# Kernel optimization log

Measured on AMD Instinct MI355X. Metric: run time of the kernel, lower is better.

The kernel has to match this reference:

```python
import jax, jax.numpy as jnp
import numpy as np

EPS = 1e-6

def elu_feature_map(x):
    return jax.nn.elu(x) + 1.0

def setup_inputs() -> dict:
    key = jax.random.key(0)
    kq, kk, kv = jax.random.split(key, 3)
    N, L, S, H, D = 8, 8192, 8192, 8, 32
    queries = jax.random.normal(kq, (N, L, H, D), dtype=jnp.float32)
    keys = jax.random.normal(kk, (N, S, H, D), dtype=jnp.float32)
    values = jax.random.normal(kv, (N, S, H, D), dtype=jnp.float32)
    return {"queries": queries, "keys": keys, "values": values}

def reference(queries, keys, values):
    # Linear attention ("Transformers are RNNs"), ELU+1 feature map.
    Q = elu_feature_map(queries)            # [N, L, H, D]
    K = elu_feature_map(keys)               # [N, S, H, D]
    v_length = values.shape[1]
    v = values / v_length                   # [N, S, H, D]
    # KV = sum_s K_s (outer) V_s  -> [N, H, D, D] (fused, no per-token outer products)
    KV = jnp.einsum('nshd,nshv->nhdv', K, v)
    # Normalizer: Z = 1 / (Q . sum_s K_s + eps)  -> [N, L, H]
    K_sum = K.sum(axis=1)                   # [N, H, D]
    Z = 1.0 / (jnp.einsum('nlhd,nhd->nlh', Q, K_sum) + EPS)
    # out = (Q @ KV) * Z * v_length  -> [N, L, H, D]
    out = jnp.einsum('nlhd,nhdv->nlhv', Q, KV) * Z[..., None] * v_length
    return out
```

## Files before the change

### kernel.cpp

```cpp
#include <hip/hip_runtime.h>
#include <hip/hip_bf16.h>


#define NN 8
#define LL 8192
#define SS 8192
#define HH 8
#define DD 32
#define HD (HH*DD)
#define EPSF 1e-6f

#define KV_FLOATS (NN*HH*DD*DD)
#define KS_FLOATS (NN*HH*DD)
#define FINAL_FLOATS (KV_FLOATS + KS_FLOATS)

#define P1_CHUNKS 64
#define P1_BLOCKS (NN*P1_CHUNKS)
#define P1_CS (SS/P1_CHUNKS)
#define P1_TS 8
#define PBLK 8448

#define P2_TS 8
#define P2_LB 64
#define P2_CHUNKS (LL/P2_LB)

__device__ __forceinline__ float elu1(float x) {
    return x > 0.f ? x + 1.f : __expf(x);
}

template<bool ATOMIC>
__global__ __launch_bounds__(512)
void la_phase1(const float* __restrict__ keys, const float* __restrict__ values,
               float* __restrict__ outbuf) {
    __shared__ float lK[P1_TS*HD];
    __shared__ float lV[P1_TS*HD];
    const int t = threadIdx.x;
    const int b = blockIdx.x;
    const int n = b / P1_CHUNKS;
    const int s0 = (b % P1_CHUNKS) * P1_CS;
    const int vh = t >> 8;
    const int h = (t >> 5) & 7;
    const int d = t & 31;

    const float4* Kg = (const float4*)(keys + ((size_t)n*SS + s0) * HD);
    const float4* Vg = (const float4*)(values + ((size_t)n*SS + s0) * HD);
    float4* lK4 = (float4*)lK;
    float4* lV4 = (float4*)lV;

    float acc[16];
#pragma unroll
    for (int i = 0; i < 16; ++i) acc[i] = 0.f;
    float ks = 0.f;

    float4 kreg = Kg[t];
    float4 vreg = Vg[t];

    for (int si = 0; si < P1_CS; si += P1_TS) {
        kreg.x = elu1(kreg.x); kreg.y = elu1(kreg.y);
        kreg.z = elu1(kreg.z); kreg.w = elu1(kreg.w);
        __syncthreads();
        lK4[t] = kreg;
        lV4[t] = vreg;
        __syncthreads();
        if (si + P1_TS < P1_CS) {
            kreg = Kg[(si + P1_TS)*(HD/4) + t];
            vreg = Vg[(si + P1_TS)*(HD/4) + t];
        }
        const float* lVb = lV + h*DD + vh*16;
#pragma unroll
        for (int i = 0; i < P1_TS; ++i) {
            const float kv = lK[i*HD + h*DD + d];
            ks += kv;
            const float4* vp = (const float4*)(lVb + i*HD);
#pragma unroll
            for (int j4 = 0; j4 < 4; ++j4) {
                const float4 vv = vp[j4];
                acc[j4*4+0] = fmaf(kv, vv.x, acc[j4*4+0]);
                acc[j4*4+1] = fmaf(kv, vv.y, acc[j4*4+1]);
                acc[j4*4+2] = fmaf(kv, vv.z, acc[j4*4+2]);
                acc[j4*4+3] = fmaf(kv, vv.w, acc[j4*4+3]);
            }
        }
    }

    if (ATOMIC) {
        float* kvdst = outbuf + ((size_t)(n*HH + h)*DD + d)*DD + vh*16;
#pragma unroll
        for (int j = 0; j < 16; ++j) atomicAdd(kvdst + j, acc[j]);
        if (vh == 0) atomicAdd(outbuf + KV_FLOATS + (n*HH + h)*DD + d, ks);
    } else {
        float* pb = outbuf + (size_t)b * PBLK;
        float4* kvdst = (float4*)(pb + (h*DD + d)*DD + vh*16);
#pragma unroll
        for (int j4 = 0; j4 < 4; ++j4)
            kvdst[j4] = make_float4(acc[j4*4+0], acc[j4*4+1], acc[j4*4+2], acc[j4*4+3]);
        if (vh == 0) pb[8192 + h*DD + d] = ks;
    }
}

__global__ __launch_bounds__(256)
void la_reduce(const float* __restrict__ part, float* __restrict__ finalbuf) {
    const int o = blockIdx.x * 256 + threadIdx.x;
    const int n = o / PBLK;
    const int e = o - n * PBLK;
    const float* p = part + (size_t)(n * P1_CHUNKS) * PBLK + e;
    float s = 0.f;
#pragma unroll 8
    for (int c = 0; c < P1_CHUNKS; ++c) s += p[(size_t)c * PBLK];
    if (e < HH*DD*DD) finalbuf[(size_t)n*(HH*DD*DD) + e] = s;
    else              finalbuf[KV_FLOATS + n*HD + (e - HH*DD*DD)] = s;
}

__global__ __launch_bounds__(256)
void la_phase2(const float* __restrict__ queries, const float* __restrict__ finalbuf,
               float* __restrict__ out) {
    __shared__ float lKV[HH*DD*DD];
    __shared__ float lQ[P2_TS*HD];
    const int t = threadIdx.x;
    const int b = blockIdx.x;
    const int n = b / P2_CHUNKS;
    const int l0 = (b % P2_CHUNKS) * P2_LB;

    const float4* kvg = (const float4*)(finalbuf + (size_t)n * (HH*DD*DD));
    float4* lKV4 = (float4*)lKV;
#pragma unroll
    for (int i = 0; i < 8; ++i) lKV4[t + i*256] = kvg[t + i*256];

    const int hA  = (t >> 3) & 7;
    const int d4A = t & 7;
    const int i2  = t >> 6;
    const int r   = t & 63;
    const int hC  = r >> 3;
    const int v4C = r & 7;

    const float4 ksA = ((const float4*)(finalbuf + KV_FLOATS + (size_t)n*HD))[hA*8 + d4A];

    const float4* Qg = (const float4*)(queries + ((size_t)n*LL + l0) * HD);
    float4 q[2];
    q[0] = Qg[t];
    q[1] = Qg[t + 256];

    __syncthreads();

    for (int li = 0; li < P2_LB; li += P2_TS) {
        float zp[2];
#pragma unroll
        for (int c = 0; c < 2; ++c) {
            q[c].x = elu1(q[c].x); q[c].y = elu1(q[c].y);
            q[c].z = elu1(q[c].z); q[c].w = elu1(q[c].w);
            float zz = q[c].x*ksA.x + q[c].y*ksA.y + q[c].z*ksA.z + q[c].w*ksA.w;
            zz += __shfl_xor(zz, 1);
            zz += __shfl_xor(zz, 2);
            zz += __shfl_xor(zz, 4);
            zp[c] = zz;
        }
        __syncthreads();
        ((float4*)lQ)[t]       = q[0];
        ((float4*)lQ)[t + 256] = q[1];
        __syncthreads();
        if (li + P2_TS < P2_LB) {
            q[0] = Qg[(li + P2_TS)*(HD/4) + t];
            q[1] = Qg[(li + P2_TS)*(HD/4) + t + 256];
        }

        float4 y[2];
        y[0] = make_float4(0.f,0.f,0.f,0.f);
        y[1] = make_float4(0.f,0.f,0.f,0.f);
        const float* kvb = lKV + hC*(DD*DD);
#pragma unroll
        for (int d4 = 0; d4 < 8; ++d4) {
            float4 qv0 = *(const float4*)(lQ + (i2    )*HD + hC*DD + d4*4);
            float4 qv1 = *(const float4*)(lQ + (i2 + 4)*HD + hC*DD + d4*4);
#pragma unroll
            for (int j = 0; j < 4; ++j) {
                const float4 kvv = *(const float4*)(kvb + (d4*4 + j)*DD + v4C*4);
                const float q0 = (&qv0.x)[j];
                const float q1 = (&qv1.x)[j];
                y[0].x = fmaf(q0, kvv.x, y[0].x);
                y[0].y = fmaf(q0, kvv.y, y[0].y);
                y[0].z = fmaf(q0, kvv.z, y[0].z);
                y[0].w = fmaf(q0, kvv.w, y[0].w);
                y[1].x = fmaf(q1, kvv.x, y[1].x);
                y[1].y = fmaf(q1, kvv.y, y[1].y);
                y[1].z = fmaf(q1, kvv.z, y[1].z);
                y[1].w = fmaf(q1, kvv.w, y[1].w);
            }
        }
#pragma unroll
        for (int k = 0; k < 2; ++k) {
            const float zs = __shfl(zp[k], hC * 8);
            const float z = 1.0f / (zs + EPSF);
            float4 yy = y[k];
            yy.x *= z; yy.y *= z; yy.z *= z; yy.w *= z;
            const int l = l0 + li + i2 + 4*k;
            float4* dst = (float4*)(out + ((size_t)n*LL + l)*HD + hC*DD);
            dst[v4C] = yy;
        }
    }
}

extern "C" void kernel_launch(void* const* d_in, const int* in_sizes, int n_in,
                              void* d_out, int out_size, void* d_ws, size_t ws_size,
                              hipStream_t stream) {
    const float* q = (const float*)d_in[0];
    const float* k = (const float*)d_in[1];
    const float* v = (const float*)d_in[2];
    float* out = (float*)d_out;

    const size_t partial_floats = (size_t)P1_BLOCKS * PBLK;
    const size_t need = (partial_floats + FINAL_FLOATS) * sizeof(float);

    if (ws_size >= need) {
        float* part = (float*)d_ws;
        float* fin  = part + partial_floats;
        la_phase1<false><<<dim3(P1_BLOCKS), dim3(512), 0, stream>>>(k, v, part);
        la_reduce<<<dim3(FINAL_FLOATS/256), dim3(256), 0, stream>>>(part, fin);
        la_phase2<<<dim3(NN*P2_CHUNKS), dim3(256), 0, stream>>>(q, fin, out);
    } else {
        float* fin = (float*)d_ws;
        hipMemsetAsync(fin, 0, FINAL_FLOATS*sizeof(float), stream);
        la_phase1<true><<<dim3(P1_BLOCKS), dim3(512), 0, stream>>>(k, v, fin);
        la_phase2<<<dim3(NN*P2_CHUNKS), dim3(256), 0, stream>>>(q, fin, out);
    }
}
```

Baseline: 234.5 us.

## Register-tile both phases with larger per-thread outer-product blocks

Phase 1 moves to 256 threads, each accumulating an 8x4 block of the KV outer product from float4 LDS reads, and stages 16 tokens per sync. Phase 2 is restructured so each block handles 128 queries for two heads. It stores ELU(Q) transposed with an XOR swizzle in LDS and computes a 4x8 output tile per thread, with the normalizer dot product fused into the same loop. The aim is a lower LDS-load-to-FMA ratio and fewer barriers, at the cost of more registers and less contiguous Q loads.

```diff
diff --git a/kernel.cpp b/kernel.cpp
--- a/kernel.cpp
+++ b/kernel.cpp
@@ -1,5 +1,4 @@
 #include <hip/hip_runtime.h>
-#include <hip/hip_bf16.h>
 
 
 #define NN 8
@@ -7,94 +6,100 @@
 #define SS 8192
 #define HH 8
 #define DD 32
-#define HD (HH*DD)
+#define HD 256
 #define EPSF 1e-6f
 
 #define KV_FLOATS (NN*HH*DD*DD)
-#define KS_FLOATS (NN*HH*DD)
-#define FINAL_FLOATS (KV_FLOATS + KS_FLOATS)
+#define FINAL_FLOATS (KV_FLOATS + NN*HH*DD)
 
 #define P1_CHUNKS 64
 #define P1_BLOCKS (NN*P1_CHUNKS)
 #define P1_CS (SS/P1_CHUNKS)
-#define P1_TS 8
+#define P1_TS 16
 #define PBLK 8448
 
-#define P2_TS 8
-#define P2_LB 64
-#define P2_CHUNKS (LL/P2_LB)
+#define P2_I 128
+#define P2_BLOCKS (NN*4*(LL/P2_I))
 
 __device__ __forceinline__ float elu1(float x) {
     return x > 0.f ? x + 1.f : __expf(x);
 }
+#define ELU4(v) { v.x = elu1(v.x); v.y = elu1(v.y); v.z = elu1(v.z); v.w = elu1(v.w); }
 
 template<bool ATOMIC>
-__global__ __launch_bounds__(512)
+__global__ __launch_bounds__(256)
 void la_phase1(const float* __restrict__ keys, const float* __restrict__ values,
                float* __restrict__ outbuf) {
-    __shared__ float lK[P1_TS*HD];
-    __shared__ float lV[P1_TS*HD];
+    __shared__ float4 lK4[P1_TS*64];
+    __shared__ float4 lV4[P1_TS*64];
     const int t = threadIdx.x;
     const int b = blockIdx.x;
     const int n = b / P1_CHUNKS;
     const int s0 = (b % P1_CHUNKS) * P1_CS;
-    const int vh = t >> 8;
-    const int h = (t >> 5) & 7;
-    const int d = t & 31;
-
-    const float4* Kg = (const float4*)(keys + ((size_t)n*SS + s0) * HD);
-    const float4* Vg = (const float4*)(values + ((size_t)n*SS + s0) * HD);
-    float4* lK4 = (float4*)lK;
-    float4* lV4 = (float4*)lV;
-
-    float acc[16];
-#pragma unroll
-    for (int i = 0; i < 16; ++i) acc[i] = 0.f;
-    float ks = 0.f;
-
-    float4 kreg = Kg[t];
-    float4 vreg = Vg[t];
+    const int h  = t >> 5;
+    const int dO = (t >> 3) & 3;
+    const int vO = t & 7;
+
+    const float4* Kg = (const float4*)(keys   + ((size_t)n*SS + s0)*HD);
+    const float4* Vg = (const float4*)(values + ((size_t)n*SS + s0)*HD);
+
+    float4 acc[8];
+#pragma unroll
+    for (int i = 0; i < 8; ++i) acc[i] = make_float4(0.f,0.f,0.f,0.f);
+    float4 ksa = make_float4(0.f,0.f,0.f,0.f), ksb = make_float4(0.f,0.f,0.f,0.f);
+
+    float4 kp[4], vp[4];
+#pragma unroll
+    for (int r = 0; r < 4; ++r) { kp[r] = Kg[t + 256*r]; vp[r] = Vg[t + 256*r]; }
+
+    const int kbase = h*8 + dO*2;
+    const int vbase = h*8 + vO;
 
     for (int si = 0; si < P1_CS; si += P1_TS) {
-        kreg.x = elu1(kreg.x); kreg.y = elu1(kreg.y);
-        kreg.z = elu1(kreg.z); kreg.w = elu1(kreg.w);
+#pragma unroll
+        for (int r = 0; r < 4; ++r) ELU4(kp[r]);
         __syncthreads();
-        lK4[t] = kreg;
-        lV4[t] = vreg;
+#pragma unroll
+        for (int r = 0; r < 4; ++r) { lK4[t + 256*r] = kp[r]; lV4[t + 256*r] = vp[r]; }
         __syncthreads();
         if (si + P1_TS < P1_CS) {
-            kreg = Kg[(si + P1_TS)*(HD/4) + t];
-            vreg = Vg[(si + P1_TS)*(HD/4) + t];
-        }
-        const float* lVb = lV + h*DD + vh*16;
+            const int nb = (si + P1_TS) * 64;
+#pragma unroll
+            for (int r = 0; r < 4; ++r) { kp[r] = Kg[nb + t + 256*r]; vp[r] = Vg[nb + t + 256*r]; }
+        }
 #pragma unroll
         for (int i = 0; i < P1_TS; ++i) {
-            const float kv = lK[i*HD + h*DD + d];
-            ks += kv;
-            const float4* vp = (const float4*)(lVb + i*HD);
-#pragma unroll
-            for (int j4 = 0; j4 < 4; ++j4) {
-                const float4 vv = vp[j4];
-                acc[j4*4+0] = fmaf(kv, vv.x, acc[j4*4+0]);
-                acc[j4*4+1] = fmaf(kv, vv.y, acc[j4*4+1]);
-                acc[j4*4+2] = fmaf(kv, vv.z, acc[j4*4+2]);
-                acc[j4*4+3] = fmaf(kv, vv.w, acc[j4*4+3]);
-            }
+            const float4 k0 = lK4[i*64 + kbase];
+            const float4 k1 = lK4[i*64 + kbase + 1];
+            const float4 vv = lV4[i*64 + vbase];
+            ksa.x += k0.x; ksa.y += k0.y; ksa.z += k0.z; ksa.w += k0.w;
+            ksb.x += k1.x; ksb.y += k1.y; ksb.z += k1.z; ksb.w += k1.w;
+#define P1F(A,S) A.x=fmaf(S,vv.x,A.x); A.y=fmaf(S,vv.y,A.y); A.z=fmaf(S,vv.z,A.z); A.w=fmaf(S,vv.w,A.w);
+            P1F(acc[0],k0.x) P1F(acc[1],k0.y) P1F(acc[2],k0.z) P1F(acc[3],k0.w)
+            P1F(acc[4],k1.x) P1F(acc[5],k1.y) P1F(acc[6],k1.z) P1F(acc[7],k1.w)
+#undef P1F
         }
     }
 
     if (ATOMIC) {
-        float* kvdst = outbuf + ((size_t)(n*HH + h)*DD + d)*DD + vh*16;
-#pragma unroll
-        for (int j = 0; j < 16; ++j) atomicAdd(kvdst + j, acc[j]);
-        if (vh == 0) atomicAdd(outbuf + KV_FLOATS + (n*HH + h)*DD + d, ks);
+        float* kvb = outbuf + (size_t)n*(HH*DD*DD) + h*(DD*DD) + (dO*8)*DD + vO*4;
+#pragma unroll
+        for (int dd = 0; dd < 8; ++dd) {
+            atomicAdd(kvb + dd*DD + 0, acc[dd].x);
+            atomicAdd(kvb + dd*DD + 1, acc[dd].y);
+            atomicAdd(kvb + dd*DD + 2, acc[dd].z);
+            atomicAdd(kvb + dd*DD + 3, acc[dd].w);
+        }
+        if (vO == 0) {
+            float* kb = outbuf + KV_FLOATS + n*HD + h*DD + dO*8;
+            atomicAdd(kb+0, ksa.x); atomicAdd(kb+1, ksa.y); atomicAdd(kb+2, ksa.z); atomicAdd(kb+3, ksa.w);
+            atomicAdd(kb+4, ksb.x); atomicAdd(kb+5, ksb.y); atomicAdd(kb+6, ksb.z); atomicAdd(kb+7, ksb.w);
+        }
     } else {
-        float* pb = outbuf + (size_t)b * PBLK;
-        float4* kvdst = (float4*)(pb + (h*DD + d)*DD + vh*16);
-#pragma unroll
-        for (int j4 = 0; j4 < 4; ++j4)
-            kvdst[j4] = make_float4(acc[j4*4+0], acc[j4*4+1], acc[j4*4+2], acc[j4*4+3]);
-        if (vh == 0) pb[8192 + h*DD + d] = ks;
+        float4* pb4 = (float4*)(outbuf + (size_t)b * PBLK);
+#pragma unroll
+        for (int dd = 0; dd < 8; ++dd) pb4[h*256 + (dO*8+dd)*8 + vO] = acc[dd];
+        if (vO == 0) { pb4[2048 + h*8 + dO*2] = ksa; pb4[2048 + h*8 + dO*2 + 1] = ksb; }
     }
 }
 
@@ -114,89 +119,83 @@
 __global__ __launch_bounds__(256)
 void la_phase2(const float* __restrict__ queries, const float* __restrict__ finalbuf,
                float* __restrict__ out) {
-    __shared__ float lKV[HH*DD*DD];
-    __shared__ float lQ[P2_TS*HD];
+    __shared__ float4 lqt4s[2*DD*P2_I/4];
+    __shared__ float4 lkv4[2*DD*DD/4];
+    __shared__ float4 lks4[16];
+    float* lqt = (float*)lqt4s;
+
     const int t = threadIdx.x;
     const int b = blockIdx.x;
-    const int n = b / P2_CHUNKS;
-    const int l0 = (b % P2_CHUNKS) * P2_LB;
-
-    const float4* kvg = (const float4*)(finalbuf + (size_t)n * (HH*DD*DD));
-    float4* lKV4 = (float4*)lKV;
-#pragma unroll
-    for (int i = 0; i < 8; ++i) lKV4[t + i*256] = kvg[t + i*256];
-
-    const int hA  = (t >> 3) & 7;
-    const int d4A = t & 7;
-    const int i2  = t >> 6;
-    const int r   = t & 63;
-    const int hC  = r >> 3;
-    const int v4C = r & 7;
-
-    const float4 ksA = ((const float4*)(finalbuf + KV_FLOATS + (size_t)n*HD))[hA*8 + d4A];
-
-    const float4* Qg = (const float4*)(queries + ((size_t)n*LL + l0) * HD);
-    float4 q[2];
-    q[0] = Qg[t];
-    q[1] = Qg[t + 256];
-
+    const int n  = b >> 8;
+    const int hp = (b >> 6) & 3;
+    const int l0 = (b & 63) * P2_I;
+
+    const float4* fin4 = (const float4*)finalbuf;
+    lkv4[t]       = fin4[(size_t)n*2048 + hp*512 + t];
+    lkv4[t + 256] = fin4[(size_t)n*2048 + hp*512 + t + 256];
+    if (t < 16) lks4[t] = fin4[KV_FLOATS/4 + n*64 + hp*16 + t];
+
+    const int irow = t >> 4;
+    const int shh  = (t >> 3) & 1;
+    const int d4   = t & 7;
+    const float4* Qg4 = (const float4*)queries;
+    const size_t qb = ((size_t)n*LL + l0)*64 + (size_t)(hp*16 + shh*8 + d4);
+    float* dst0 = lqt + shh*4096 + (d4*4)*P2_I;
+#pragma unroll
+    for (int k = 0; k < 8; ++k) {
+        const int i = irow + k*16;
+        float4 qv = Qg4[qb + (size_t)i*64];
+        ELU4(qv);
+        const int ip = i ^ (d4 << 2);
+        dst0[ip] = qv.x; dst0[P2_I + ip] = qv.y; dst0[2*P2_I + ip] = qv.z; dst0[3*P2_I + ip] = qv.w;
+    }
     __syncthreads();
 
-    for (int li = 0; li < P2_LB; li += P2_TS) {
-        float zp[2];
-#pragma unroll
-        for (int c = 0; c < 2; ++c) {
-            q[c].x = elu1(q[c].x); q[c].y = elu1(q[c].y);
-            q[c].z = elu1(q[c].z); q[c].w = elu1(q[c].w);
-            float zz = q[c].x*ksA.x + q[c].y*ksA.y + q[c].z*ksA.z + q[c].w*ksA.w;
-            zz += __shfl_xor(zz, 1);
-            zz += __shfl_xor(zz, 2);
-            zz += __shfl_xor(zz, 4);
-            zp[c] = zz;
-        }
-        __syncthreads();
-        ((float4*)lQ)[t]       = q[0];
-        ((float4*)lQ)[t + 256] = q[1];
-        __syncthreads();
-        if (li + P2_TS < P2_LB) {
-            q[0] = Qg[(li + P2_TS)*(HD/4) + t];
-            q[1] = Qg[(li + P2_TS)*(HD/4) + t + 256];
-        }
-
-        float4 y[2];
-        y[0] = make_float4(0.f,0.f,0.f,0.f);
-        y[1] = make_float4(0.f,0.f,0.f,0.f);
-        const float* kvb = lKV + hC*(DD*DD);
-#pragma unroll
-        for (int d4 = 0; d4 < 8; ++d4) {
-            float4 qv0 = *(const float4*)(lQ + (i2    )*HD + hC*DD + d4*4);
-            float4 qv1 = *(const float4*)(lQ + (i2 + 4)*HD + hC*DD + d4*4);
-#pragma unroll
-            for (int j = 0; j < 4; ++j) {
-                const float4 kvv = *(const float4*)(kvb + (d4*4 + j)*DD + v4C*4);
-                const float q0 = (&qv0.x)[j];
-                const float q1 = (&qv1.x)[j];
-                y[0].x = fmaf(q0, kvv.x, y[0].x);
-                y[0].y = fmaf(q0, kvv.y, y[0].y);
-                y[0].z = fmaf(q0, kvv.z, y[0].z);
-                y[0].w = fmaf(q0, kvv.w, y[0].w);
-                y[1].x = fmaf(q1, kvv.x, y[1].x);
-                y[1].y = fmaf(q1, kvv.y, y[1].y);
-                y[1].z = fmaf(q1, kvv.z, y[1].z);
-                y[1].w = fmaf(q1, kvv.w, y[1].w);
-            }
-        }
-#pragma unroll
-        for (int k = 0; k < 2; ++k) {
-            const float zs = __shfl(zp[k], hC * 8);
-            const float z = 1.0f / (zs + EPSF);
-            float4 yy = y[k];
-            yy.x *= z; yy.y *= z; yy.z *= z; yy.w *= z;
-            const int l = l0 + li + i2 + 4*k;
-            float4* dst = (float4*)(out + ((size_t)n*LL + l)*HD + hC*DD);
-            dst[v4C] = yy;
-        }
-    }
+    const int voct = t & 3;
+    const int hh   = (t >> 2) & 1;
+    const int lq   = t >> 3;
+
+    float4 a0[4], a1[4];
+#pragma unroll
+    for (int i = 0; i < 4; ++i) { a0[i] = make_float4(0.f,0.f,0.f,0.f); a1[i] = make_float4(0.f,0.f,0.f,0.f); }
+    float z0 = 0.f, z1 = 0.f, z2 = 0.f, z3 = 0.f;
+
+    const float4* lqt4 = (const float4*)lqt;
+    const int qbase  = hh*1024;
+    const int kvbase = hh*256 + voct*2;
+
+#define FMA8(L, QS) \
+    a0[L].x = fmaf(QS, kA.x, a0[L].x); a0[L].y = fmaf(QS, kA.y, a0[L].y); \
+    a0[L].z = fmaf(QS, kA.z, a0[L].z); a0[L].w = fmaf(QS, kA.w, a0[L].w); \
+    a1[L].x = fmaf(QS, kB.x, a1[L].x); a1[L].y = fmaf(QS, kB.y, a1[L].y); \
+    a1[L].z = fmaf(QS, kB.z, a1[L].z); a1[L].w = fmaf(QS, kB.w, a1[L].w);
+
+#define P2S(J, KSD) { \
+    const int d = dq*4 + (J); \
+    const float4 qv = lqt4[qbase + d*32 + (lq ^ dq)]; \
+    const float4 kA = lkv4[kvbase + d*8]; \
+    const float4 kB = lkv4[kvbase + d*8 + 1]; \
+    z0 = fmaf(qv.x, KSD, z0); z1 = fmaf(qv.y, KSD, z1); \
+    z2 = fmaf(qv.z, KSD, z2); z3 = fmaf(qv.w, KSD, z3); \
+    FMA8(0, qv.x) FMA8(1, qv.y) FMA8(2, qv.z) FMA8(3, qv.w) }
+
+#pragma unroll
+    for (int dq = 0; dq < 8; ++dq) {
+        const float4 ks = lks4[hh*8 + dq];
+        P2S(0, ks.x) P2S(1, ks.y) P2S(2, ks.z) P2S(3, ks.w)
+    }
+#undef P2S
+#undef FMA8
+
+    float4* out4 = (float4*)out;
+    const size_t ob = ((size_t)n*LL + l0 + lq*4)*64 + (size_t)(hp*16 + hh*8 + voct*2);
+#define P2OUT(L, ZV) { \
+    const float zi = 1.0f/((ZV) + EPSF); \
+    float4 r0 = a0[L], r1 = a1[L]; \
+    r0.x*=zi; r0.y*=zi; r0.z*=zi; r0.w*=zi; r1.x*=zi; r1.y*=zi; r1.z*=zi; r1.w*=zi; \
+    out4[ob + (size_t)(L)*64] = r0; out4[ob + (size_t)(L)*64 + 1] = r1; }
+    P2OUT(0, z0) P2OUT(1, z1) P2OUT(2, z2) P2OUT(3, z3)
+#undef P2OUT
 }
 
 extern "C" void kernel_launch(void* const* d_in, const int* in_sizes, int n_in,
@@ -213,13 +212,13 @@
     if (ws_size >= need) {
         float* part = (float*)d_ws;
         float* fin  = part + partial_floats;
-        la_phase1<false><<<dim3(P1_BLOCKS), dim3(512), 0, stream>>>(k, v, part);
+        la_phase1<false><<<dim3(P1_BLOCKS), dim3(256), 0, stream>>>(k, v, part);
         la_reduce<<<dim3(FINAL_FLOATS/256), dim3(256), 0, stream>>>(part, fin);
-        la_phase2<<<dim3(NN*P2_CHUNKS), dim3(256), 0, stream>>>(q, fin, out);
+        la_phase2<<<dim3(P2_BLOCKS), dim3(256), 0, stream>>>(q, fin, out);
     } else {
         float* fin = (float*)d_ws;
         hipMemsetAsync(fin, 0, FINAL_FLOATS*sizeof(float), stream);
-        la_phase1<true><<<dim3(P1_BLOCKS), dim3(512), 0, stream>>>(k, v, fin);
-        la_phase2<<<dim3(NN*P2_CHUNKS), dim3(256), 0, stream>>>(q, fin, out);
-    }
-}
+        la_phase1<true><<<dim3(P1_BLOCKS), dim3(256), 0, stream>>>(k, v, fin);
+        la_phase2<<<dim3(P2_BLOCKS), dim3(256), 0, stream>>>(q, fin, out);
+    }
+}
```

Measured after the change: 242.9 us. +3.6%, slower.
